# Performance work log

Hardware: AMD Instinct MI355X
Metric: run time of the kernel (lower is better)

Reference implementation:

```python
import jax, jax.numpy as jnp
import numpy as np

C_I, C_T, NUM_HEADS = 128, 256, 8
EPS = 1e-5

def conv3d1(x, W, b):
    # 1x1x1 conv: x (b,c,D,H,W), W (o,c), b (o,)
    return jnp.einsum('oc,bcdhw->bodhw', W, x) + b[None, :, None, None, None]

def conv1d1(x, W, b):
    # kernel_size=1 conv: x (b,c,l), W (o,c), b (o,)
    return jnp.einsum('oc,bcl->bol', W, x) + b[None, :, None]

def inorm3d(x):
    # InstanceNorm3d(affine=False): normalize over spatial dims, biased var
    m = jnp.mean(x, axis=(2, 3, 4), keepdims=True)
    v = jnp.var(x, axis=(2, 3, 4), keepdims=True)
    return (x - m) * jax.lax.rsqrt(v + EPS)

def setup_inputs() -> dict:
    key = jax.random.key(0)
    ks = jax.random.split(key, 20)
    B, D, H, W, L = 2, 48, 48, 48, 20
    s = 0.05
    inp = {
        'img_in': jax.random.normal(ks[0], (B, C_I, D, H, W), jnp.float32),
        'lang_in': jax.random.normal(ks[1], (B, C_T, L), jnp.float32),
        'Wq': jax.random.normal(ks[2], (C_I, C_I), jnp.float32) * s,
        'bq': jnp.zeros((C_I,), jnp.float32),
        'Wk': jax.random.normal(ks[3], (C_I, C_T), jnp.float32) * s,
        'bk': jnp.zeros((C_I,), jnp.float32),
        'Wv': jax.random.normal(ks[4], (C_I, C_T), jnp.float32) * s,
        'bv': jnp.zeros((C_I,), jnp.float32),
        'Wpw': jax.random.normal(ks[5], (C_I, C_I), jnp.float32) * s,
        'bpw': jnp.zeros((C_I,), jnp.float32),
        'Wpi': jax.random.normal(ks[6], (C_I, C_I), jnp.float32) * s,
        'bpi': jnp.zeros((C_I,), jnp.float32),
        'Wpo': jax.random.normal(ks[7], (C_I, C_I), jnp.float32) * s,
        'bpo': jnp.zeros((C_I,), jnp.float32),
        'Wg1': jax.random.normal(ks[8], (C_I, C_I), jnp.float32) * s,
        'bg1': jnp.zeros((C_I,), jnp.float32),
        'Wg2': jax.random.normal(ks[9], (C_I, C_I), jnp.float32) * s,
        'bg2': jnp.zeros((C_I,), jnp.float32),
    }
    return inp

def reference(img_in, lang_in, Wq, bq, Wk, bk, Wv, bv, Wpw, bpw, Wpi, bpi,
              Wpo, bpo, Wg1, bg1, Wg2, bg2):
    b = img_in.shape[0]
    d = int(np.prod(img_in.shape[-3:]))
    l = lang_in.shape[-1]
    hd = C_I // NUM_HEADS
    # lang_mask=None path -> all-ones mask (additive term is zero but kept faithful)
    mask = jnp.ones((b, 1, l), img_in.dtype)

    # query: conv3d(1x1)+InstanceNorm -> (b, heads, d, hd)
    q = inorm3d(conv3d1(img_in, Wq, bq)).reshape(b, C_I, d)
    q = q.transpose(0, 2, 1).reshape(b, d, NUM_HEADS, hd).transpose(0, 2, 1, 3)
    # key/value: conv1d(k=1) masked -> (b, heads, hd, l)
    k = (conv1d1(lang_in, Wk, bk) * mask).reshape(b, NUM_HEADS, hd, l)
    v = (conv1d1(lang_in, Wv, bv) * mask).reshape(b, NUM_HEADS, hd, l)

    scale = (C_I / NUM_HEADS) ** (-0.5)
    sim = jnp.einsum('bhdc,bhcl->bhdl', q, k) * scale
    sim = sim + (10000.0 * mask[:, :, None, :] - 10000.0)  # (b,1,1,l) broadcast
    attn = jax.nn.softmax(sim, axis=-1)
    x = jnp.einsum('bhdl,bhcl->bhdc', attn, v)              # (b,heads,d,hd)
    x = x.transpose(0, 2, 1, 3).reshape(b, d, C_I)
    # faithful to torch .permute(0,2,1).permute(0,2,1).view_as(img_in):
    # reshape (b, d, c_i) flat buffer into (b, c_i, D, H, W)
    x_img = x.reshape(img_in.shape)

    skip = inorm3d(conv3d1(img_in, Wpi, bpi))
    weight = inorm3d(conv3d1(x_img, Wpw, bpw))
    out = jax.nn.relu(conv3d1(skip * weight, Wpo, bpo))
    gate = jnp.tanh(conv3d1(jax.nn.relu(conv3d1(out, Wg1, bg1)), Wg2, bg2))
    return out * gate
```

## Files before the change

### kernel.cpp

```cpp
#include <hip/hip_runtime.h>
#include <cstdint>
#include <cstddef>

#define PSP 110592
#define NCH 128
#define NB  2
#define CPW 66
#define TPB 4
static constexpr float EPSV = 1e-5f;

typedef short bf16x8 __attribute__((ext_vector_type(8)));
typedef float f32x4  __attribute__((ext_vector_type(4)));

static __device__ __forceinline__ short f2bf(float f) {
    uint32_t u = __builtin_bit_cast(uint32_t, f);
    u += 0x7FFF + ((u >> 16) & 1);
    return (short)(u >> 16);
}
static __device__ __forceinline__ float bf2f(short s) {
    uint32_t u = ((uint32_t)(uint16_t)s) << 16;
    return __builtin_bit_cast(float, u);
}
static __device__ __forceinline__ float bfLO(uint32_t w) { return bf2f((short)(w & 0xffff)); }
static __device__ __forceinline__ float bfHI(uint32_t w) { return bf2f((short)(w >> 16)); }
static __device__ __forceinline__ uint32_t pk2f(float lo, float hi) {
    return (uint32_t)(uint16_t)f2bf(lo) | ((uint32_t)(uint16_t)f2bf(hi) << 16);
}
static __device__ __forceinline__ uint32_t pk2s(short lo, short hi) {
    return (uint32_t)(uint16_t)lo | ((uint32_t)(uint16_t)hi << 16);
}

__global__ __launch_bounds__(256) void kv_kernel(
    const float* __restrict__ lang,
    const float* __restrict__ Wk, const float* __restrict__ bk,
    const float* __restrict__ Wv, const float* __restrict__ bv,
    float* __restrict__ kout, float* __restrict__ vout)
{
    int gid = blockIdx.x * 256 + threadIdx.x;
    int sel = gid / 5120;
    int r   = gid % 5120;
    int b   = r / 2560;
    int o   = (r % 2560) / 20;
    int l   = r % 20;
    const float* W  = sel ? Wv : Wk;
    const float* bb = sel ? bv : bk;
    const float* lg = lang + b * 256 * 20 + l;
    float acc = bb[o];
    #pragma unroll 8
    for (int c = 0; c < 256; ++c)
        acc = fmaf(W[o * 256 + c], lg[c * 20], acc);
    (sel ? vout : kout)[b * 2560 + o * 20 + l] = acc;
}

__global__ __launch_bounds__(256) void wprep_kernel(
    const float* __restrict__ w0, const float* __restrict__ w1,
    const float* __restrict__ w2, const float* __restrict__ w3,
    const float* __restrict__ w4, const float* __restrict__ w5,
    short* __restrict__ wt)
{
    const int m = blockIdx.x >> 4, s = blockIdx.x & 15;
    const float* src = w0;
    if (m == 1) src = w1; else if (m == 2) src = w2; else if (m == 3) src = w3;
    else if (m == 4) src = w4; else if (m == 5) src = w5;
    short* dst = wt + m * NCH * NCH;
    const int i0 = s * 1024 + threadIdx.x * 4;
    f32x4 v = *(const f32x4*)(src + i0);
    short s4[4] = {f2bf(v[0]), f2bf(v[1]), f2bf(v[2]), f2bf(v[3])};
    *(uint2*)(dst + i0) = make_uint2(
        pk2s(s4[0], s4[1]), pk2s(s4[2], s4[3]));
}

__global__ __launch_bounds__(256) void knprep_kernel(
    const float* __restrict__ qs, const float* __restrict__ qs2,
    const float* __restrict__ kbuf,
    float* __restrict__ knb, float* __restrict__ cbb)
{
    __shared__ float mq[128], rqs[128], knl[2560];
    const int t = threadIdx.x, b = blockIdx.x;
    if (t < 128) {
        float m = qs[b * 128 + t] * (1.0f / PSP);
        float v = qs2[b * 128 + t] * (1.0f / PSP) - m * m;
        mq[t] = m;
        rqs[t] = rsqrtf(v + EPSV) * 0.25f;
    }
    __syncthreads();
    for (int e = t; e < 2560; e += 256) {
        int c = e / 20;
        float kv = rqs[c] * kbuf[b * 2560 + e];
        knl[e] = kv;
        knb[b * 2560 + e] = kv;
    }
    __syncthreads();
    if (t < 160) {
        int h = t / 20, l = t % 20;
        float s = 0.0f;
        #pragma unroll
        for (int i = 0; i < 16; ++i)
            s = fmaf(mq[h * 16 + i], knl[(h * 16 + i) * 20 + l], s);
        cbb[b * 160 + t] = s;
    }
}

struct RawF32 { f32x4 a[4], b[4]; };
struct RawB16 { bf16x8 a0, a1, b0, b1; };

static __device__ __forceinline__ void ld_raw_f32(const float* src, RawF32& r) {
    const int t = threadIdx.x;
    const float* s0 = src + (size_t)(2 * (t >> 2)) * PSP + (t & 3) * 16;
    #pragma unroll
    for (int i = 0; i < 4; ++i) {
        r.a[i] = *(const f32x4*)(s0 + i * 4);
        r.b[i] = *(const f32x4*)(s0 + PSP + i * 4);
    }
}
static __device__ __forceinline__ void st_f32(uint32_t* STG, const RawF32& r) {
    const int t = threadIdx.x;
    uint32_t w[16];
    #pragma unroll
    for (int i = 0; i < 4; ++i)
        #pragma unroll
        for (int j = 0; j < 4; ++j) w[i * 4 + j] = pk2f(r.a[i][j], r.b[i][j]);
    uint32_t* base = STG + (t >> 2) * CPW + (t & 3) * 16;
    #pragma unroll
    for (int k = 0; k < 8; ++k) *(uint2*)(base + 2 * k) = make_uint2(w[2 * k], w[2 * k + 1]);
}
static __device__ __forceinline__ void ld_raw_b16(const short* src, RawB16& r) {
    const int t = threadIdx.x;
    const short* s0 = src + (size_t)(2 * (t >> 2)) * PSP + (t & 3) * 16;
    r.a0 = *(const bf16x8*)s0;         r.a1 = *(const bf16x8*)(s0 + 8);
    r.b0 = *(const bf16x8*)(s0 + PSP); r.b1 = *(const bf16x8*)(s0 + PSP + 8);
}
static __device__ __forceinline__ void st_b16(uint32_t* STG, const RawB16& r) {
    const int t = threadIdx.x;
    uint32_t w[16];
    #pragma unroll
    for (int k = 0; k < 8; ++k) { w[k] = pk2s(r.a0[k], r.b0[k]); w[8 + k] = pk2s(r.a1[k], r.b1[k]); }
    uint32_t* base = STG + (t >> 2) * CPW + (t & 3) * 16;
    #pragma unroll
    for (int k = 0; k < 8; ++k) *(uint2*)(base + 2 * k) = make_uint2(w[2 * k], w[2 * k + 1]);
}
static __device__ __forceinline__ void st_g4(uint32_t* STG, const RawB16& rs, const RawB16& rw,
                                             const float nm[4][NCH]) {
    const int t = threadIdx.x;
    const int c = 2 * (t >> 2);
    const float mA0 = nm[0][c], rA0 = nm[1][c], mA1 = nm[0][c+1], rA1 = nm[1][c+1];
    const float mB0 = nm[2][c], rB0 = nm[3][c], mB1 = nm[2][c+1], rB1 = nm[3][c+1];
    uint32_t w[16];
    #pragma unroll
    for (int k = 0; k < 8; ++k) {
        float lo  = ((bf2f(rs.a0[k]) - mA0) * rA0) * ((bf2f(rw.a0[k]) - mB0) * rB0);
        float hi  = ((bf2f(rs.b0[k]) - mA1) * rA1) * ((bf2f(rw.b0[k]) - mB1) * rB1);
        float lo2 = ((bf2f(rs.a1[k]) - mA0) * rA0) * ((bf2f(rw.a1[k]) - mB0) * rB0);
        float hi2 = ((bf2f(rs.b1[k]) - mA1) * rA1) * ((bf2f(rw.b1[k]) - mB1) * rB1);
        w[k] = pk2f(lo, hi); w[8 + k] = pk2f(lo2, hi2);
    }
    uint32_t* base = STG + (t >> 2) * CPW + (t & 3) * 16;
    #pragma unroll
    for (int k = 0; k < 8; ++k) *(uint2*)(base + 2 * k) = make_uint2(w[2 * k], w[2 * k + 1]);
}

static __device__ __forceinline__ void load_afrag16(const short* __restrict__ W16,
                                                    int wid, int lane, bf16x8 af[2][4]) {
    const int orow = wid * 32 + (lane & 15);
    const int cb   = (lane >> 4) * 8;
    #pragma unroll
    for (int mt = 0; mt < 2; ++mt)
        #pragma unroll
        for (int kt = 0; kt < 4; ++kt)
            af[mt][kt] = *(const bf16x8*)(W16 + (size_t)(orow + mt * 16) * NCH + kt * 32 + cb);
}

static __device__ __forceinline__ bf16x8 read_bfrag(const uint32_t* CP, int c2b, int p) {
    union { uint32_t u[4]; bf16x8 f; } cv;
    #pragma unroll
    for (int i = 0; i < 4; ++i) cv.u[i] = CP[(c2b + i) * CPW + p];
    return cv.f;
}
static __device__ __forceinline__ void run_mfma(const uint32_t* CP, const bf16x8 af[2][4],
                                                f32x4 acc[2][4], int lane) {
    const int l15 = lane & 15, kh = lane >> 4;
    #pragma unroll
    for (int nt = 0; nt < 4; ++nt) {
        const int p = nt * 16 + l15;
        bf16x8 bf[4];
        #pragma unroll
        for (int kt = 0; kt < 4; ++kt) bf[kt] = read_bfrag(CP, kt * 16 + kh * 4, p);
        #pragma unroll
        for (int kt = 0; kt < 4; ++kt) {
            acc[0][nt] = __builtin_amdgcn_mfma_f32_16x16x32_bf16(af[0][kt], bf[kt], acc[0][nt], 0, 0, 0);
            acc[1][nt] = __builtin_amdgcn_mfma_f32_16x16x32_bf16(af[1][kt], bf[kt], acc[1][nt], 0, 0, 0);
        }
    }
}
static __device__ __forceinline__ void zero_acc(f32x4 acc[2][4]) {
    #pragma unroll
    for (int m = 0; m < 2; ++m)
        #pragma unroll
        for (int n = 0; n < 4; ++n) acc[m][n] = (f32x4)0.0f;
}
static __device__ __forceinline__ void write_LCp(uint32_t* LCp, const f32x4 acc[2][4],
                                                 int wid, int lane) {
    const int l15 = lane & 15, og = wid * 32 + (lane >> 4) * 4;
    #pragma unroll
    for (int mt = 0; mt < 2; ++mt)
        #pragma unroll
        for (int nt = 0; nt < 4; ++nt) {
            const int o2 = (og >> 1) + mt * 8, p = nt * 16 + l15;
            f32x4 a = acc[mt][nt];
            LCp[o2 * CPW + p]       = pk2f(a[0], a[1]);
            LCp[(o2 + 1) * CPW + p] = pk2f(a[2], a[3]);
        }
}
template<bool RELU, bool STATS>
static __device__ __forceinline__ void epi_store(const uint32_t* LCp, const float* __restrict__ bias,
        short* __restrict__ dst, float* sredS, float* sredQ)
{
    const int t = threadIdx.x;
    #pragma unroll
    for (int r = 0; r < 4; ++r) {
        const int u = r * 256 + t, o = u >> 3, ch = u & 7, hi = o & 1;
        const float bia = bias[o];
        const uint32_t* src = LCp + (o >> 1) * CPW + ch * 8;
        float v[8];
        #pragma unroll
        for (int j = 0; j < 4; ++j) {
            uint2 ww = *(const uint2*)(src + 2 * j);
            v[2*j]   = (hi ? bfHI(ww.x) : bfLO(ww.x)) + bia;
            v[2*j+1] = (hi ? bfHI(ww.y) : bfLO(ww.y)) + bia;
        }
        if (RELU) {
            #pragma unroll
            for (int j = 0; j < 8; ++j) v[j] = fmaxf(v[j], 0.0f);
        }
        bf16x8 s8;
        #pragma unroll
        for (int j = 0; j < 8; ++j) s8[j] = f2bf(v[j]);
        *(bf16x8*)(dst + (size_t)o * PSP + ch * 8) = s8;
        if (STATS) {
            float s = 0.0f, q = 0.0f;
            #pragma unroll
            for (int j = 0; j < 8; ++j) { s += v[j]; q += v[j] * v[j]; }
            s += __shfl_xor(s, 1); q += __shfl_xor(q, 1);
            s += __shfl_xor(s, 2); q += __shfl_xor(q, 2);
            s += __shfl_xor(s, 4); q += __shfl_xor(q, 4);
            if ((t & 7) == 0) { sredS[o] = s; sredQ[o] = q; }
        }
    }
}

__global__ __launch_bounds__(256) void g12_kernel(
    const float* __restrict__ img, const short* __restrict__ w16,
    const float* __restrict__ bq, const float* __restrict__ bpi,
    short* __restrict__ qout, short* __restrict__ sout,
    float* __restrict__ qs, float* __restrict__ qs2,
    float* __restrict__ ss, float* __restrict__ ss2)
{
    __shared__ __align__(16) uint32_t STG[2][64 * CPW];
    __shared__ __align__(16) uint32_t LCp[64 * CPW];
    __shared__ float sredS[128], sredQ[128];

    const int t = threadIdx.x, lane = t & 63, wid = t >> 6;
    const int b = blockIdx.y;
    const size_t bbase = (size_t)b * NCH * PSP;
    const int pbase = blockIdx.x * (64 * TPB);
    const int sb = b * NCH;

    bf16x8 afq[2][4], afp[2][4];
    load_afrag16(w16, wid, lane, afq);
    load_afrag16(w16 + NCH * NCH, wid, lane, afp);

    RawF32 rw;
    ld_raw_f32(img + bbase + pbase, rw);
    st_f32(STG[0], rw);
    __syncthreads();

    for (int i = 0; i < TPB; ++i) {
        const int cur = i & 1, nxt = cur ^ 1;
        const int pblk = pbase + i * 64;
        if (i + 1 < TPB) ld_raw_f32(img + bbase + pblk + 64, rw);
        f32x4 acc[2][4];
        zero_acc(acc);
        run_mfma(STG[cur], afq, acc, lane);
        __syncthreads();
        if (i + 1 < TPB) st_f32(STG[nxt], rw);
        write_LCp(LCp, acc, wid, lane);
        __syncthreads();
        zero_acc(acc);
        run_mfma(STG[cur], afp, acc, lane);
        epi_store<false, true>(LCp, bq, qout + bbase + pblk, sredS, sredQ);
        __syncthreads();
        if (t < 128) { atomicAdd(&qs[sb + t], sredS[t]); atomicAdd(&qs2[sb + t], sredQ[t]); }
        write_LCp(LCp, acc, wid, lane);
        __syncthreads();
        epi_store<false, true>(LCp, bpi, sout + bbase + pblk, sredS, sredQ);
        __syncthreads();
        if (t < 128) { atomicAdd(&ss[sb + t], sredS[t]); atomicAdd(&ss2[sb + t], sredQ[t]); }
    }
}

__global__ __launch_bounds__(256) void g3_kernel(
    const short* __restrict__ x, const short* __restrict__ w16,
    const float* __restrict__ bpw, short* __restrict__ wout,
    float* __restrict__ wsu, float* __restrict__ ws2)
{
    __shared__ __align__(16) uint32_t STG[2][64 * CPW];
    __shared__ __align__(16) uint32_t LCp[64 * CPW];
    __shared__ float sredS[128], sredQ[128];

    const int t = threadIdx.x, lane = t & 63, wid = t >> 6;
    const int b = blockIdx.y;
    const size_t bbase = (size_t)b * NCH * PSP;
    const int pbase = blockIdx.x * (64 * TPB);
    const int sb = b * NCH;

    bf16x8 af[2][4];
    load_afrag16(w16, wid, lane, af);

    RawB16 rw;
    ld_raw_b16(x + bbase + pbase, rw);
    st_b16(STG[0], rw);
    __syncthreads();

    for (int i = 0; i < TPB; ++i) {
        const int cur = i & 1, nxt = cur ^ 1;
        const int pblk = pbase + i * 64;
        if (i + 1 < TPB) ld_raw_b16(x + bbase + pblk + 64, rw);
        f32x4 acc[2][4];
        zero_acc(acc);
        run_mfma(STG[cur], af, acc, lane);
        __syncthreads();
        if (i + 1 < TPB) st_b16(STG[nxt], rw);
        write_LCp(LCp, acc, wid, lane);
        __syncthreads();
        epi_store<false, true>(LCp, bpw, wout + bbase + pblk, sredS, sredQ);
        __syncthreads();
        if (t < 128) { atomicAdd(&wsu[sb + t], sredS[t]); atomicAdd(&ws2[sb + t], sredQ[t]); }
    }
}

__global__ __launch_bounds__(256) void g4_kernel(
    const short* __restrict__ skip, const short* __restrict__ wgt,
    const float* __restrict__ sA, const float* __restrict__ sA2,
    const float* __restrict__ sB, const float* __restrict__ sB2,
    const short* __restrict__ w16, const float* __restrict__ bpo,
    short* __restrict__ outp)
{
    __shared__ __align__(16) uint32_t STG[2][64 * CPW];
    __shared__ __align__(16) uint32_t LCp[64 * CPW];
    __shared__ float nm[4][NCH];

    const int t = threadIdx.x, lane = t & 63, wid = t >> 6;
    const int b = blockIdx.y;
    const size_t bbase = (size_t)b * NCH * PSP;
    const int pbase = blockIdx.x * (64 * TPB);

    if (t < NCH) {
        float m = sA[b * NCH + t] * (1.0f / PSP);
        float v = sA2[b * NCH + t] * (1.0f / PSP) - m * m;
        nm[0][t] = m; nm[1][t] = rsqrtf(v + EPSV);
    } else {
        int c = t - NCH;
        float m = sB[b * NCH + c] * (1.0f / PSP);
        float v = sB2[b * NCH + c] * (1.0f / PSP) - m * m;
        nm[2][c] = m; nm[3][c] = rsqrtf(v + EPSV);
    }

    bf16x8 af[2][4];
    load_afrag16(w16, wid, lane, af);

    RawB16 rs, rw;
    ld_raw_b16(skip + bbase + pbase, rs);
    ld_raw_b16(wgt  + bbase + pbase, rw);
    __syncthreads();
    st_g4(STG[0], rs, rw, nm);
    __syncthreads();

    for (int i = 0; i < TPB; ++i) {
        const int cur = i & 1, nxt = cur ^ 1;
        const int pblk = pbase + i * 64;
        if (i + 1 < TPB) {
            ld_raw_b16(skip + bbase + pblk + 64, rs);
            ld_raw_b16(wgt  + bbase + pblk + 64, rw);
        }
        f32x4 acc[2][4];
        zero_acc(acc);
        run_mfma(STG[cur], af, acc, lane);
        __syncthreads();
        if (i + 1 < TPB) st_g4(STG[nxt], rs, rw, nm);
        write_LCp(LCp, acc, wid, lane);
        __syncthreads();
        epi_store<true, false>(LCp, bpo, outp + bbase + pblk, nullptr, nullptr);
    }
}

__global__ __launch_bounds__(256) void g56_kernel(
    const short* __restrict__ outb, const short* __restrict__ w16g1,
    const float* __restrict__ bg1, const short* __restrict__ w16g2,
    const float* __restrict__ bg2, float* __restrict__ fin)
{
    __shared__ __align__(16) uint32_t STG[2][64 * CPW];
    __shared__ __align__(16) uint32_t RT[64 * CPW];

    const int t = threadIdx.x, lane = t & 63, wid = t >> 6;
    const int b = blockIdx.y;
    const size_t bbase = (size_t)b * NCH * PSP;
    const int pbase = blockIdx.x * (64 * TPB);

    bf16x8 af1[2][4], af2[2][4];
    load_afrag16(w16g1, wid, lane, af1);
    load_afrag16(w16g2, wid, lane, af2);

    float bg1v[2][4];
    {
        const int og = wid * 32 + (lane >> 4) * 4;
        #pragma unroll
        for (int mt = 0; mt < 2; ++mt)
            #pragma unroll
            for (int r = 0; r < 4; ++r) bg1v[mt][r] = bg1[og + mt * 16 + r];
    }

    RawB16 rw;
    ld_raw_b16(outb + bbase + pbase, rw);
    st_b16(STG[0], rw);
    __syncthreads();

    for (int i = 0; i < TPB; ++i) {
        const int cur = i & 1, nxt = cur ^ 1;
        const int pblk = pbase + i * 64;
        if (i + 1 < TPB) ld_raw_b16(outb + bbase + pblk + 64, rw);
        f32x4 acc[2][4];
        zero_acc(acc);
        run_mfma(STG[cur], af1, acc, lane);
        __syncthreads();
        {
            const int l15 = lane & 15, og = wid * 32 + (lane >> 4) * 4;
            #pragma unroll
            for (int mt = 0; mt < 2; ++mt)
                #pragma unroll
                for (int nt = 0; nt < 4; ++nt) {
                    const int o2 = (og >> 1) + mt * 8, p = nt * 16 + l15;
                    f32x4 a = acc[mt][nt];
                    float z0 = fmaxf(a[0] + bg1v[mt][0], 0.0f);
                    float z1 = fmaxf(a[1] + bg1v[mt][1], 0.0f);
                    float z2 = fmaxf(a[2] + bg1v[mt][2], 0.0f);
                    float z3 = fmaxf(a[3] + bg1v[mt][3], 0.0f);
                    RT[o2 * CPW + p]       = pk2f(z0, z1);
                    RT[(o2 + 1) * CPW + p] = pk2f(z2, z3);
                }
        }
        if (i + 1 < TPB) st_b16(STG[nxt], rw);
        __syncthreads();
        zero_acc(acc);
        run_mfma(RT, af2, acc, lane);
        __syncthreads();
        write_LCp(RT, acc, wid, lane);
        __syncthreads();
        {
            float* dst = fin + bbase + pblk;
            #pragma unroll
            for (int r = 0; r < 8; ++r) {
                const int u = r * 256 + t, o = u >> 4, ch = u & 15, hi = o & 1;
                const float bia = bg2[o];
                const uint32_t* lc = RT + (o >> 1) * CPW + ch * 4;
                const uint32_t* mg = STG[cur] + (o >> 1) * CPW + ch * 4;
                uint2 l0 = *(const uint2*)lc, l1 = *(const uint2*)(lc + 2);
                uint2 m0 = *(const uint2*)mg, m1 = *(const uint2*)(mg + 2);
                f32x4 ov;
                ov[0] = (hi ? bfHI(m0.x) : bfLO(m0.x)) * tanhf((hi ? bfHI(l0.x) : bfLO(l0.x)) + bia);
                ov[1] = (hi ? bfHI(m0.y) : bfLO(m0.y)) * tanhf((hi ? bfHI(l0.y) : bfLO(l0.y)) + bia);
                ov[2] = (hi ? bfHI(m1.x) : bfLO(m1.x)) * tanhf((hi ? bfHI(l1.x) : bfLO(l1.x)) + bia);
                ov[3] = (hi ? bfHI(m1.y) : bfLO(m1.y)) * tanhf((hi ? bfHI(l1.y) : bfLO(l1.y)) + bia);
                *(f32x4*)(dst + (size_t)o * PSP + ch * 4) = ov;
            }
        }
        __syncthreads();
    }
}

__global__ __launch_bounds__(256) void attn3_kernel(
    const short* __restrict__ qpre, const float* __restrict__ knb,
    const float* __restrict__ cbb, const float* __restrict__ vbuf,
    short* __restrict__ xout)
{
    __shared__ __align__(16) uint32_t QX[64 * 65];
    __shared__ float KN[2560], VV[2560], CB[160];

    const int t = threadIdx.x;
    const int b = blockIdx.y;
    const int pblk = blockIdx.x * 64;
    const size_t bbase = (size_t)b * NCH * PSP;

    {
        const float* kn = knb + b * 2560;
        const float* vv = vbuf + b * 2560;
        #pragma unroll
        for (int e = t; e < 2560; e += 256) { KN[e] = kn[e]; VV[e] = vv[e]; }
        if (t < 160) CB[t] = cbb[b * 160 + t];
    }
    {
        const int c2 = t >> 2, p0 = (t & 3) * 16;
        const short* s0 = qpre + bbase + (size_t)(2 * c2) * PSP + pblk + p0;
        bf16x8 a0 = *(const bf16x8*)s0,         a1 = *(const bf16x8*)(s0 + 8);
        bf16x8 b0 = *(const bf16x8*)(s0 + PSP), b1 = *(const bf16x8*)(s0 + PSP + 8);
        uint32_t w[16];
        #pragma unroll
        for (int k = 0; k < 8; ++k) { w[k] = pk2s(a0[k], b0[k]); w[8 + k] = pk2s(a1[k], b1[k]); }
        uint32_t* base = QX + c2 * 65 + p0;
        #pragma unroll
        for (int k = 0; k < 8; ++k) *(uint2*)(base + 2 * k) = make_uint2(w[2 * k], w[2 * k + 1]);
    }
    __syncthreads();

    const int p = t & 63, h0 = t >> 6;
    uint32_t qw[16];
    #pragma unroll
    for (int i = 0; i < 8; ++i) {
        qw[i]     = QX[(h0 * 8 + i) * 65 + p];
        qw[8 + i] = QX[((h0 + 4) * 8 + i) * 65 + p];
    }
    __syncthreads();

    #pragma unroll 1
    for (int hh = 0; hh < 2; ++hh) {
        const int h = h0 + hh * 4;
        const int c0 = h * 16;
        float sim[20];
        #pragma unroll
        for (int l = 0; l < 20; ++l) sim[l] = -CB[h * 20 + l];
        #pragma unroll
        for (int i = 0; i < 8; ++i) {
            const uint32_t w = qw[hh * 8 + i];
            const float qlo = bfLO(w), qhi = bfHI(w);
            const float* k0 = KN + (c0 + 2 * i) * 20;
            #pragma unroll
            for (int l = 0; l < 20; ++l)
                sim[l] = fmaf(qlo, k0[l], fmaf(qhi, k0[20 + l], sim[l]));
        }
        float mx = sim[0];
        #pragma unroll
        for (int l = 1; l < 20; ++l) mx = fmaxf(mx, sim[l]);
        float se = 0.0f;
        #pragma unroll
        for (int l = 0; l < 20; ++l) { float e = __expf(sim[l] - mx); sim[l] = e; se += e; }
        const float inv = 1.0f / se;
        #pragma unroll
        for (int i = 0; i < 8; ++i) {
            const float* v0 = VV + (c0 + 2 * i) * 20;
            float x0 = 0.0f, x1 = 0.0f;
            #pragma unroll
            for (int l = 0; l < 20; ++l) {
                x0 = fmaf(sim[l], v0[l], x0);
                x1 = fmaf(sim[l], v0[20 + l], x1);
            }
            QX[p * 65 + h * 8 + i] = pk2f(x0 * inv, x1 * inv);
        }
    }
    __syncthreads();

    {
        const int lane = t & 63, w = t >> 6;
        uint32_t* gdst = (uint32_t*)(xout + bbase + (size_t)pblk * NCH);
        #pragma unroll
        for (int j = 0; j < 4; ++j) {
            const int pp = w * 4 + j * 16 + (lane >> 4);
            const int cw = (lane & 15) * 4;
            const uint32_t* s = QX + pp * 65 + cw;
            *(uint4*)(gdst + pp * 64 + cw) = make_uint4(s[0], s[1], s[2], s[3]);
        }
    }
}

extern "C" void kernel_launch(void* const* d_in, const int* in_sizes, int n_in,
                              void* d_out, int out_size, void* d_ws, size_t ws_size,
                              hipStream_t stream)
{
    const float* img  = (const float*)d_in[0];
    const float* lang = (const float*)d_in[1];
    const float* Wq   = (const float*)d_in[2];
    const float* bq   = (const float*)d_in[3];
    const float* Wk   = (const float*)d_in[4];
    const float* bk   = (const float*)d_in[5];
    const float* Wv   = (const float*)d_in[6];
    const float* bv   = (const float*)d_in[7];
    const float* Wpw  = (const float*)d_in[8];
    const float* bpw  = (const float*)d_in[9];
    const float* Wpi  = (const float*)d_in[10];
    const float* bpi  = (const float*)d_in[11];
    const float* Wpo  = (const float*)d_in[12];
    const float* bpo  = (const float*)d_in[13];
    const float* Wg1  = (const float*)d_in[14];
    const float* bg1  = (const float*)d_in[15];
    const float* Wg2  = (const float*)d_in[16];
    const float* bg2  = (const float*)d_in[17];
    float* outp = (float*)d_out;

    const size_t N = (size_t)NB * NCH * PSP;
    const size_t needed = 3 * N * sizeof(short) + 6 * NCH * NCH * sizeof(short)
                        + (3 * 2 * 2560 + 2 * 160 + 6 * 256) * sizeof(float);
    if (ws_size < needed) return;

    short* bufA = (short*)d_ws;
    short* bufB = bufA + N;
    short* bufC = bufB + N;
    short* wt16 = bufC + N;
    float* kbuf = (float*)(wt16 + 6 * NCH * NCH);
    float* vbuf = kbuf + 2 * 2560;
    float* knb  = vbuf + 2 * 2560;
    float* cbb  = knb + 2 * 2560;
    float* st   = cbb + 2 * 160;
    float* qs   = st;
    float* qs2  = st + 256;
    float* ss   = st + 512;
    float* ss2  = st + 768;
    float* wsu  = st + 1024;
    float* ws2  = st + 1280;

    hipMemsetAsync(st, 0, 6 * 256 * sizeof(float), stream);
    kv_kernel<<<dim3(40), dim3(256), 0, stream>>>(lang, Wk, bk, Wv, bv, kbuf, vbuf);
    wprep_kernel<<<dim3(96), dim3(256), 0, stream>>>(Wq, Wpi, Wpw, Wpo, Wg1, Wg2, wt16);

    const dim3 gg(PSP / (64 * TPB), NB), gb(256);

    g12_kernel<<<gg, gb, 0, stream>>>(img, wt16, bq, bpi, bufA, bufC, qs, qs2, ss, ss2);
    knprep_kernel<<<dim3(NB), dim3(256), 0, stream>>>(qs, qs2, kbuf, knb, cbb);
    attn3_kernel<<<dim3(PSP / 64, NB), gb, 0, stream>>>(bufA, knb, cbb, vbuf, bufB);
    g3_kernel<<<gg, gb, 0, stream>>>(bufB, wt16 + 2 * NCH * NCH, bpw, bufA, wsu, ws2);
    g4_kernel<<<gg, gb, 0, stream>>>(bufC, bufA, ss, ss2, wsu, ws2,
                                     wt16 + 3 * NCH * NCH, bpo, bufB);
    g56_kernel<<<gg, gb, 0, stream>>>(bufB, wt16 + 4 * NCH * NCH, bg1,
                                      wt16 + 5 * NCH * NCH, bg2, outp);
}
```

Before: 359.0 us.

## Switch staging to swizzled pixel-major LDS layout and accumulate stats in registers

```diff
diff --git a/kernel.cpp b/kernel.cpp
--- a/kernel.cpp
+++ b/kernel.cpp
@@ -5,7 +5,7 @@
 #define PSP 110592
 #define NCH 128
 #define NB  2
-#define CPW 66
+#define CPW 68
 #define TPB 4
 static constexpr float EPSV = 1e-5f;
 
@@ -28,6 +28,9 @@
 }
 static __device__ __forceinline__ uint32_t pk2s(short lo, short hi) {
     return (uint32_t)(uint16_t)lo | ((uint32_t)(uint16_t)hi << 16);
+}
+static __device__ __forceinline__ int swzb(int p) {
+    return (((p & 7) ^ ((p >> 3) & 7)) << 4);
 }
 
 __global__ __launch_bounds__(256) void kv_kernel(
@@ -65,9 +68,8 @@
     short* dst = wt + m * NCH * NCH;
     const int i0 = s * 1024 + threadIdx.x * 4;
     f32x4 v = *(const f32x4*)(src + i0);
-    short s4[4] = {f2bf(v[0]), f2bf(v[1]), f2bf(v[2]), f2bf(v[3])};
-    *(uint2*)(dst + i0) = make_uint2(
-        pk2s(s4[0], s4[1]), pk2s(s4[2], s4[3]));
+    *(uint2*)(dst + i0) = make_uint2(pk2f(v[0], v[1]) ,
+                                     pk2f(v[2], v[3]));
 }
 
 __global__ __launch_bounds__(256) void knprep_kernel(
@@ -101,62 +103,68 @@
     }
 }
 
-struct RawF32 { f32x4 a[4], b[4]; };
-struct RawB16 { bf16x8 a0, a1, b0, b1; };
-
-static __device__ __forceinline__ void ld_raw_f32(const float* src, RawF32& r) {
+struct PackW { uint32_t lo[8], hi[8]; };
+
+static __device__ __forceinline__ void ldpack_f32(const float* src, PackW& w) {
     const int t = threadIdx.x;
-    const float* s0 = src + (size_t)(2 * (t >> 2)) * PSP + (t & 3) * 16;
-    #pragma unroll
-    for (int i = 0; i < 4; ++i) {
-        r.a[i] = *(const f32x4*)(s0 + i * 4);
-        r.b[i] = *(const f32x4*)(s0 + PSP + i * 4);
-    }
-}
-static __device__ __forceinline__ void st_f32(uint32_t* STG, const RawF32& r) {
+    const float* s = src + (size_t)(4 * (t >> 3)) * PSP + (t & 7) * 8;
+    f32x4 r0a = *(const f32x4*)s,             r0b = *(const f32x4*)(s + 4);
+    f32x4 r1a = *(const f32x4*)(s + PSP),     r1b = *(const f32x4*)(s + PSP + 4);
+    f32x4 r2a = *(const f32x4*)(s + 2 * PSP), r2b = *(const f32x4*)(s + 2 * PSP + 4);
+    f32x4 r3a = *(const f32x4*)(s + 3 * PSP), r3b = *(const f32x4*)(s + 3 * PSP + 4);
+    #pragma unroll
+    for (int j = 0; j < 4; ++j) {
+        w.lo[j]     = pk2f(r0a[j], r1a[j]);
+        w.lo[4 + j] = pk2f(r0b[j], r1b[j]);
+        w.hi[j]     = pk2f(r2a[j], r3a[j]);
+        w.hi[4 + j] = pk2f(r2b[j], r3b[j]);
+    }
+}
+static __device__ __forceinline__ void ldpack_b16(const short* src, PackW& w) {
     const int t = threadIdx.x;
-    uint32_t w[16];
-    #pragma unroll
-    for (int i = 0; i < 4; ++i)
-        #pragma unroll
-        for (int j = 0; j < 4; ++j) w[i * 4 + j] = pk2f(r.a[i][j], r.b[i][j]);
-    uint32_t* base = STG + (t >> 2) * CPW + (t & 3) * 16;
-    #pragma unroll
-    for (int k = 0; k < 8; ++k) *(uint2*)(base + 2 * k) = make_uint2(w[2 * k], w[2 * k + 1]);
-}
-static __device__ __forceinline__ void ld_raw_b16(const short* src, RawB16& r) {
+    const short* s = src + (size_t)(4 * (t >> 3)) * PSP + (t & 7) * 8;
+    bf16x8 r0 = *(const bf16x8*)s;
+    bf16x8 r1 = *(const bf16x8*)(s + PSP);
+    bf16x8 r2 = *(const bf16x8*)(s + 2 * PSP);
+    bf16x8 r3 = *(const bf16x8*)(s + 3 * PSP);
+    #pragma unroll
+    for (int j = 0; j < 8; ++j) { w.lo[j] = pk2s(r0[j], r1[j]); w.hi[j] = pk2s(r2[j], r3[j]); }
+}
+static __device__ __forceinline__ void ldpack_g4(const short* skip, const short* wgt,
+        const float nm[4][NCH], PackW& w) {
     const int t = threadIdx.x;
-    const short* s0 = src + (size_t)(2 * (t >> 2)) * PSP + (t & 3) * 16;
-    r.a0 = *(const bf16x8*)s0;         r.a1 = *(const bf16x8*)(s0 + 8);
-    r.b0 = *(const bf16x8*)(s0 + PSP); r.b1 = *(const bf16x8*)(s0 + PSP + 8);
-}
-static __device__ __forceinline__ void st_b16(uint32_t* STG, const RawB16& r) {
+    const int c = 4 * (t >> 3), p0 = (t & 7) * 8;
+    const short* s = skip + (size_t)c * PSP + p0;
+    const short* g = wgt  + (size_t)c * PSP + p0;
+    bf16x8 s0 = *(const bf16x8*)s,             s1 = *(const bf16x8*)(s + PSP);
+    bf16x8 s2 = *(const bf16x8*)(s + 2 * PSP), s3 = *(const bf16x8*)(s + 3 * PSP);
+    bf16x8 g0 = *(const bf16x8*)g,             g1 = *(const bf16x8*)(g + PSP);
+    bf16x8 g2 = *(const bf16x8*)(g + 2 * PSP), g3 = *(const bf16x8*)(g + 3 * PSP);
+    float mA[4], rA[4], mB[4], rB[4];
+    #pragma unroll
+    for (int r = 0; r < 4; ++r) {
+        mA[r] = nm[0][c + r]; rA[r] = nm[1][c + r];
+        mB[r] = nm[2][c + r]; rB[r] = nm[3][c + r];
+    }
+    #pragma unroll
+    for (int j = 0; j < 8; ++j) {
+        float v0 = ((bf2f(s0[j]) - mA[0]) * rA[0]) * ((bf2f(g0[j]) - mB[0]) * rB[0]);
+        float v1 = ((bf2f(s1[j]) - mA[1]) * rA[1]) * ((bf2f(g1[j]) - mB[1]) * rB[1]);
+        float v2 = ((bf2f(s2[j]) - mA[2]) * rA[2]) * ((bf2f(g2[j]) - mB[2]) * rB[2]);
+        float v3 = ((bf2f(s3[j]) - mA[3]) * rA[3]) * ((bf2f(g3[j]) - mB[3]) * rB[3]);
+        w.lo[j] = pk2f(v0, v1);
+        w.hi[j] = pk2f(v2, v3);
+    }
+}
+static __device__ __forceinline__ void stage(char* STGb, const PackW& w) {
     const int t = threadIdx.x;
-    uint32_t w[16];
-    #pragma unroll
-    for (int k = 0; k < 8; ++k) { w[k] = pk2s(r.a0[k], r.b0[k]); w[8 + k] = pk2s(r.a1[k], r.b1[k]); }
-    uint32_t* base = STG + (t >> 2) * CPW + (t & 3) * 16;
-    #pragma unroll
-    for (int k = 0; k < 8; ++k) *(uint2*)(base + 2 * k) = make_uint2(w[2 * k], w[2 * k + 1]);
-}
-static __device__ __forceinline__ void st_g4(uint32_t* STG, const RawB16& rs, const RawB16& rw,
-                                             const float nm[4][NCH]) {
-    const int t = threadIdx.x;
-    const int c = 2 * (t >> 2);
-    const float mA0 = nm[0][c], rA0 = nm[1][c], mA1 = nm[0][c+1], rA1 = nm[1][c+1];
-    const float mB0 = nm[2][c], rB0 = nm[3][c], mB1 = nm[2][c+1], rB1 = nm[3][c+1];
-    uint32_t w[16];
-    #pragma unroll
-    for (int k = 0; k < 8; ++k) {
-        float lo  = ((bf2f(rs.a0[k]) - mA0) * rA0) * ((bf2f(rw.a0[k]) - mB0) * rB0);
-        float hi  = ((bf2f(rs.b0[k]) - mA1) * rA1) * ((bf2f(rw.b0[k]) - mB1) * rB1);
-        float lo2 = ((bf2f(rs.a1[k]) - mA0) * rA0) * ((bf2f(rw.a1[k]) - mB0) * rB0);
-        float hi2 = ((bf2f(rs.b1[k]) - mA1) * rA1) * ((bf2f(rw.b1[k]) - mB1) * rB1);
-        w[k] = pk2f(lo, hi); w[8 + k] = pk2f(lo2, hi2);
-    }
-    uint32_t* base = STG + (t >> 2) * CPW + (t & 3) * 16;
-    #pragma unroll
-    for (int k = 0; k < 8; ++k) *(uint2*)(base + 2 * k) = make_uint2(w[2 * k], w[2 * k + 1]);
+    const int c8 = (t >> 3) * 8, p0 = (t & 7) * 8;
+    #pragma unroll
+    for (int j = 0; j < 8; ++j) {
+        int byte = (p0 + j) * 256 + c8;
+        byte ^= ((j ^ (t & 7)) << 4);
+        *(uint2*)(STGb + byte) = make_uint2(w.lo[j], w.hi[j]);
+    }
 }
 
 static __device__ __forceinline__ void load_afrag16(const short* __restrict__ W16,
@@ -170,21 +178,17 @@
             af[mt][kt] = *(const bf16x8*)(W16 + (size_t)(orow + mt * 16) * NCH + kt * 32 + cb);
 }
 
-static __device__ __forceinline__ bf16x8 read_bfrag(const uint32_t* CP, int c2b, int p) {
-    union { uint32_t u[4]; bf16x8 f; } cv;
-    #pragma unroll
-    for (int i = 0; i < 4; ++i) cv.u[i] = CP[(c2b + i) * CPW + p];
-    return cv.f;
-}
-static __device__ __forceinline__ void run_mfma(const uint32_t* CP, const bf16x8 af[2][4],
-                                                f32x4 acc[2][4], int lane) {
+static __device__ __forceinline__ void run_mfmaX(const char* STGb, const bf16x8 af[2][4],
+                                                 f32x4 acc[2][4], int lane) {
     const int l15 = lane & 15, kh = lane >> 4;
     #pragma unroll
     for (int nt = 0; nt < 4; ++nt) {
         const int p = nt * 16 + l15;
+        const int sw = swzb(p);
         bf16x8 bf[4];
         #pragma unroll
-        for (int kt = 0; kt < 4; ++kt) bf[kt] = read_bfrag(CP, kt * 16 + kh * 4, p);
+        for (int kt = 0; kt < 4; ++kt)
+            bf[kt] = *(const bf16x8*)(STGb + ((p * 256 + kt * 64 + kh * 16) ^ sw));
         #pragma unroll
         for (int kt = 0; kt < 4; ++kt) {
             acc[0][nt] = __builtin_amdgcn_mfma_f32_16x16x32_bf16(af[0][kt], bf[kt], acc[0][nt], 0, 0, 0);
@@ -212,8 +216,8 @@
         }
 }
 template<bool RELU, bool STATS>
-static __device__ __forceinline__ void epi_store(const uint32_t* LCp, const float* __restrict__ bias,
-        short* __restrict__ dst, float* sredS, float* sredQ)
+static __device__ __forceinline__ void epi2(const uint32_t* LCp, const float* __restrict__ bias,
+        short* __restrict__ dst, float sS[4], float sQ[4])
 {
     const int t = threadIdx.x;
     #pragma unroll
@@ -221,13 +225,12 @@
         const int u = r * 256 + t, o = u >> 3, ch = u & 7, hi = o & 1;
         const float bia = bias[o];
         const uint32_t* src = LCp + (o >> 1) * CPW + ch * 8;
+        uint4 wa = *(const uint4*)src;
+        uint4 wb = *(const uint4*)(src + 4);
+        uint32_t ww[8] = {wa.x, wa.y, wa.z, wa.w, wb.x, wb.y, wb.z, wb.w};
         float v[8];
         #pragma unroll
-        for (int j = 0; j < 4; ++j) {
-            uint2 ww = *(const uint2*)(src + 2 * j);
-            v[2*j]   = (hi ? bfHI(ww.x) : bfLO(ww.x)) + bia;
-            v[2*j+1] = (hi ? bfHI(ww.y) : bfLO(ww.y)) + bia;
-        }
+        for (int j = 0; j < 8; ++j) v[j] = (hi ? bfHI(ww[j]) : bfLO(ww[j])) + bia;
         if (RELU) {
             #pragma unroll
             for (int j = 0; j < 8; ++j) v[j] = fmaxf(v[j], 0.0f);
@@ -240,10 +243,23 @@
             float s = 0.0f, q = 0.0f;
             #pragma unroll
             for (int j = 0; j < 8; ++j) { s += v[j]; q += v[j] * v[j]; }
-            s += __shfl_xor(s, 1); q += __shfl_xor(q, 1);
-            s += __shfl_xor(s, 2); q += __shfl_xor(q, 2);
-            s += __shfl_xor(s, 4); q += __shfl_xor(q, 4);
-            if ((t & 7) == 0) { sredS[o] = s; sredQ[o] = q; }
+            sS[r] += s; sQ[r] += q;
+        }
+    }
+}
+static __device__ __forceinline__ void flush_stats(const float sS[4], const float sQ[4],
+        float* __restrict__ s_sum, float* __restrict__ s_sq)
+{
+    const int t = threadIdx.x;
+    #pragma unroll
+    for (int r = 0; r < 4; ++r) {
+        float s = sS[r], q = sQ[r];
+        s += __shfl_xor(s, 1); q += __shfl_xor(q, 1);
+        s += __shfl_xor(s, 2); q += __shfl_xor(q, 2);
+        s += __shfl_xor(s, 4); q += __shfl_xor(q, 4);
+        if ((t & 7) == 0) {
+            atomicAdd(&s_sum[r * 32 + (t >> 3)], s);
+            atomicAdd(&s_sq [r * 32 + (t >> 3)], q);
         }
     }
 }
@@ -255,9 +271,8 @@
     float* __restrict__ qs, float* __restrict__ qs2,
     float* __restrict__ ss, float* __restrict__ ss2)
 {
-    __shared__ __align__(16) uint32_t STG[2][64 * CPW];
+    __shared__ __align__(16) char STGb[16384];
     __shared__ __align__(16) uint32_t LCp[64 * CPW];
-    __shared__ float sredS[128], sredQ[128];
 
     const int t = threadIdx.x, lane = t & 63, wid = t >> 6;
     const int b = blockIdx.y;
@@ -269,33 +284,32 @@
     load_afrag16(w16, wid, lane, afq);
     load_afrag16(w16 + NCH * NCH, wid, lane, afp);
 
-    RawF32 rw;
-    ld_raw_f32(img + bbase + pbase, rw);
-    st_f32(STG[0], rw);
-    __syncthreads();
+    float qS[4] = {0, 0, 0, 0}, qQ[4] = {0, 0, 0, 0};
+    float sS[4] = {0, 0, 0, 0}, sQ[4] = {0, 0, 0, 0};
+
+    PackW w;
+    ldpack_f32(img + bbase + pbase, w);
 
     for (int i = 0; i < TPB; ++i) {
-        const int cur = i & 1, nxt = cur ^ 1;
         const int pblk = pbase + i * 64;
-        if (i + 1 < TPB) ld_raw_f32(img + bbase + pblk + 64, rw);
+        stage(STGb, w);
+        __syncthreads();
+        if (i + 1 < TPB) ldpack_f32(img + bbase + pblk + 64, w);
         f32x4 acc[2][4];
         zero_acc(acc);
-        run_mfma(STG[cur], afq, acc, lane);
-        __syncthreads();
-        if (i + 1 < TPB) st_f32(STG[nxt], rw);
+        run_mfmaX(STGb, afq, acc, lane);
         write_LCp(LCp, acc, wid, lane);
         __syncthreads();
+        epi2<false, true>(LCp, bq, qout + bbase + pblk, qS, qQ);
         zero_acc(acc);
-        run_mfma(STG[cur], afp, acc, lane);
-        epi_store<false, true>(LCp, bq, qout + bbase + pblk, sredS, sredQ);
-        __syncthreads();
-        if (t < 128) { atomicAdd(&qs[sb + t], sredS[t]); atomicAdd(&qs2[sb + t], sredQ[t]); }
+        run_mfmaX(STGb, afp, acc, lane);
+        __syncthreads();
         write_LCp(LCp, acc, wid, lane);
         __syncthreads();
-        epi_store<false, true>(LCp, bpi, sout + bbase + pblk, sredS, sredQ);
-        __syncthreads();
-        if (t < 128) { atomicAdd(&ss[sb + t], sredS[t]); atomicAdd(&ss2[sb + t], sredQ[t]); }
-    }
+        epi2<false, true>(LCp, bpi, sout + bbase + pblk, sS, sQ);
+    }
+    flush_stats(qS, qQ, qs + sb, qs2 + sb);
+    flush_stats(sS, sQ, ss + sb, ss2 + sb);
 }
 
 __global__ __launch_bounds__(256) void g3_kernel(
@@ -303,9 +317,8 @@
     const float* __restrict__ bpw, short* __restrict__ wout,
     float* __restrict__ wsu, float* __restrict__ ws2)
 {
-    __shared__ __align__(16) uint32_t STG[2][64 * CPW];
+    __shared__ __align__(16) char STGb[16384];
     __shared__ __align__(16) uint32_t LCp[64 * CPW];
-    __shared__ float sredS[128], sredQ[128];
 
     const int t = threadIdx.x, lane = t & 63, wid = t >> 6;
     const int b = blockIdx.y;
@@ -315,27 +328,24 @@
 
     bf16x8 af[2][4];
     load_afrag16(w16, wid, lane, af);
-
-    RawB16 rw;
-    ld_raw_b16(x + bbase + pbase, rw);
-    st_b16(STG[0], rw);
-    __syncthreads();
+    float wS[4] = {0, 0, 0, 0}, wQ[4] = {0, 0, 0, 0};
+
+    PackW w;
+    ldpack_b16(x + bbase + pbase, w);
 
     for (int i = 0; i < TPB; ++i) {
-        const int cur = i & 1, nxt = cur ^ 1;
         const int pblk = pbase + i * 64;
-        if (i + 1 < TPB) ld_raw_b16(x + bbase + pblk + 64, rw);
+        stage(STGb, w);
+        __syncthreads();
+        if (i + 1 < TPB) ldpack_b16(x + bbase + pblk + 64, w);
         f32x4 acc[2][4];
         zero_acc(acc);
-        run_mfma(STG[cur], af, acc, lane);
-        __syncthreads();
-        if (i + 1 < TPB) st_b16(STG[nxt], rw);
+        run_mfmaX(STGb, af, acc, lane);
         write_LCp(LCp, acc, wid, lane);
         __syncthreads();
-        epi_store<false, true>(LCp, bpw, wout + bbase + pblk, sredS, sredQ);
-        __syncthreads();
-        if (t < 128) { atomicAdd(&wsu[sb + t], sredS[t]); atomicAdd(&ws2[sb + t], sredQ[t]); }
-    }
+        epi2<false, true>(LCp, bpw, wout + bbase + pblk, wS, wQ);
+    }
+    flush_stats(wS, wQ, wsu + sb, ws2 + sb);
 }
 
 __global__ __launch_bounds__(256) void g4_kernel(
@@ -345,7 +355,7 @@
     const short* __restrict__ w16, const float* __restrict__ bpo,
     short* __restrict__ outp)
 {
-    __shared__ __align__(16) uint32_t STG[2][64 * CPW];
+    __shared__ __align__(16) char STGb[16384];
     __shared__ __align__(16) uint32_t LCp[64 * CPW];
     __shared__ float nm[4][NCH];
 
@@ -364,32 +374,26 @@
         float v = sB2[b * NCH + c] * (1.0f / PSP) - m * m;
         nm[2][c] = m; nm[3][c] = rsqrtf(v + EPSV);
     }
-
     bf16x8 af[2][4];
     load_afrag16(w16, wid, lane, af);
-
-    RawB16 rs, rw;
-    ld_raw_b16(skip + bbase + pbase, rs);
-    ld_raw_b16(wgt  + bbase + pbase, rw);
     __syncthreads();
-    st_g4(STG[0], rs, rw, nm);
-    __syncthreads();
+
+    PackW w;
+    ldpack_g4(skip + bbase + pbase, wgt + bbase + pbase, nm, w);
+    float dS[4], dQ[4];
 
     for (int i = 0; i < TPB; ++i) {
-        const int cur = i & 1, nxt = cur ^ 1;
         const int pblk = pbase + i * 64;
-        if (i + 1 < TPB) {
-            ld_raw_b16(skip + bbase + pblk + 64, rs);
-            ld_raw_b16(wgt  + bbase + pblk + 64, rw);
-        }
+        stage(STGb, w);
+        __syncthreads();
+        if (i + 1 < TPB)
+            ldpack_g4(skip + bbase + pblk + 64, wgt + bbase + pblk + 64, nm, w);
         f32x4 acc[2][4];
         zero_acc(acc);
-        run_mfma(STG[cur], af, acc, lane);
-        __syncthreads();
-        if (i + 1 < TPB) st_g4(STG[nxt], rs, rw, nm);
+        run_mfmaX(STGb, af, acc, lane);
         write_LCp(LCp, acc, wid, lane);
         __syncthreads();
-        epi_store<true, false>(LCp, bpo, outp + bbase + pblk, nullptr, nullptr);
+        epi2<true, false>(LCp, bpo, outp + bbase + pblk, dS, dQ);
     }
 }
 
@@ -398,8 +402,8 @@
     const float* __restrict__ bg1, const short* __restrict__ w16g2,
     const float* __restrict__ bg2, float* __restrict__ fin)
 {
-    __shared__ __align__(16) uint32_t STG[2][64 * CPW];
-    __shared__ __align__(16) uint32_t RT[64 * CPW];
+    __shared__ __align__(16) char STGb[16384];
+    __shared__ __align__(16) char RTL[64 * CPW * 4];
 
     const int t = threadIdx.x, lane = t & 63, wid = t >> 6;
     const int b = blockIdx.y;
@@ -419,58 +423,59 @@
             for (int r = 0; r < 4; ++r) bg1v[mt][r] = bg1[og + mt * 16 + r];
     }
 
-    RawB16 rw;
-    ld_raw_b16(outb + bbase + pbase, rw);
-    st_b16(STG[0], rw);
-    __syncthreads();
+    PackW w;
+    ldpack_b16(outb + bbase + pbase, w);
 
     for (int i = 0; i < TPB; ++i) {
-        const int cur = i & 1, nxt = cur ^ 1;
         const int pblk = pbase + i * 64;
-        if (i + 1 < TPB) ld_raw_b16(outb + bbase + pblk + 64, rw);
+        stage(STGb, w);
+        __syncthreads();
+        if (i + 1 < TPB) ldpack_b16(outb + bbase + pblk + 64, w);
         f32x4 acc[2][4];
         zero_acc(acc);
-        run_mfma(STG[cur], af1, acc, lane);
-        __syncthreads();
+        run_mfmaX(STGb, af1, acc, lane);
         {
             const int l15 = lane & 15, og = wid * 32 + (lane >> 4) * 4;
             #pragma unroll
             for (int mt = 0; mt < 2; ++mt)
                 #pragma unroll
                 for (int nt = 0; nt < 4; ++nt) {
-                    const int o2 = (og >> 1) + mt * 8, p = nt * 16 + l15;
+                    const int o = og + mt * 16, p = nt * 16 + l15;
+                    const int sw = swzb(p);
                     f32x4 a = acc[mt][nt];
                     float z0 = fmaxf(a[0] + bg1v[mt][0], 0.0f);
                     float z1 = fmaxf(a[1] + bg1v[mt][1], 0.0f);
                     float z2 = fmaxf(a[2] + bg1v[mt][2], 0.0f);
                     float z3 = fmaxf(a[3] + bg1v[mt][3], 0.0f);
-                    RT[o2 * CPW + p]       = pk2f(z0, z1);
-                    RT[(o2 + 1) * CPW + p] = pk2f(z2, z3);
+                    *(uint32_t*)(RTL + ((p * 256 + o * 2) ^ sw))     = pk2f(z0, z1);
+                    *(uint32_t*)(RTL + ((p * 256 + o * 2 + 4) ^ sw)) = pk2f(z2, z3);
                 }
         }
-        if (i + 1 < TPB) st_b16(STG[nxt], rw);
         __syncthreads();
         zero_acc(acc);
-        run_mfma(RT, af2, acc, lane);
-        __syncthreads();
-        write_LCp(RT, acc, wid, lane);
+        run_mfmaX(RTL, af2, acc, lane);
+        __syncthreads();
+        write_LCp((uint32_t*)RTL, acc, wid, lane);
         __syncthreads();
         {
+            const uint32_t* LCp = (const uint32_t*)RTL;
             float* dst = fin + bbase + pblk;
             #pragma unroll
-            for (int r = 0; r < 8; ++r) {
-                const int u = r * 256 + t, o = u >> 4, ch = u & 15, hi = o & 1;
-                const float bia = bg2[o];
-                const uint32_t* lc = RT + (o >> 1) * CPW + ch * 4;
-                const uint32_t* mg = STG[cur] + (o >> 1) * CPW + ch * 4;
-                uint2 l0 = *(const uint2*)lc, l1 = *(const uint2*)(lc + 2);
-                uint2 m0 = *(const uint2*)mg, m1 = *(const uint2*)(mg + 2);
-                f32x4 ov;
-                ov[0] = (hi ? bfHI(m0.x) : bfLO(m0.x)) * tanhf((hi ? bfHI(l0.x) : bfLO(l0.x)) + bia);
-                ov[1] = (hi ? bfHI(m0.y) : bfLO(m0.y)) * tanhf((hi ? bfHI(l0.y) : bfLO(l0.y)) + bia);
-                ov[2] = (hi ? bfHI(m1.x) : bfLO(m1.x)) * tanhf((hi ? bfHI(l1.x) : bfLO(l1.x)) + bia);
-                ov[3] = (hi ? bfHI(m1.y) : bfLO(m1.y)) * tanhf((hi ? bfHI(l1.y) : bfLO(l1.y)) + bia);
-                *(f32x4*)(dst + (size_t)o * PSP + ch * 4) = ov;
+            for (int r = 0; r < 4; ++r) {
+                const int u = r * 256 + t, o2 = u >> 4, ch = u & 15;
+                const float b0 = bg2[2 * o2], b1 = bg2[2 * o2 + 1];
+                uint4 lc = *(const uint4*)(LCp + o2 * CPW + ch * 4);
+                uint32_t lw[4] = {lc.x, lc.y, lc.z, lc.w};
+                f32x4 oA, oB;
+                #pragma unroll
+                for (int j = 0; j < 4; ++j) {
+                    const int p = ch * 4 + j;
+                    uint32_t mw = *(const uint32_t*)(STGb + ((p * 256 + o2 * 4) ^ swzb(p)));
+                    oA[j] = bfLO(mw) * tanhf(bfLO(lw[j]) + b0);
+                    oB[j] = bfHI(mw) * tanhf(bfHI(lw[j]) + b1);
+                }
+                *(f32x4*)(dst + (size_t)(2 * o2) * PSP + ch * 4)     = oA;
+                *(f32x4*)(dst + (size_t)(2 * o2 + 1) * PSP + ch * 4) = oB;
             }
         }
         __syncthreads();
```

Measured after the change: 322.2 us. 1.11x faster.
